# Kernel tuning notes

Measured on AMD Instinct MI355X. Metric: run time of the kernel, lower is better.

The kernel has to match this reference:

```python
import jax, jax.numpy as jnp
import numpy as np

B, S, G, E = 2048, 32768, 4096, 1024  # batch, source_size, n_groups(target_size), embeddings_size


def setup_inputs() -> dict:
    key = jax.random.key(0)
    k_x, k_w, k_we, k_perm = jax.random.split(key, 4)
    x = jax.random.normal(k_x, (B, S), dtype=jnp.float32)
    W = jax.random.normal(k_w, (E, G), dtype=jnp.float32) * 0.02  # Linear(target_size -> embed, no bias)
    # per-element weights for 'w_sum' groups (concatenated Linear(group_size,1) weights)
    w_elem = jax.random.normal(k_we, (S,), dtype=jnp.float32) * 0.1
    perm = jax.random.permutation(k_perm, S).astype(jnp.int32)
    # ragged group boundaries: n_groups groups, each size >= 1, summing to S
    rng = np.random.default_rng(0)
    cuts = np.sort(rng.choice(np.arange(1, S), G - 1, replace=False))
    sizes = np.diff(np.concatenate([[0], cuts, [S]]))
    segment_ids = jnp.asarray(np.repeat(np.arange(G), sizes), dtype=jnp.int32)
    # aggregation type per group: 0='sum', 1='or', 2='w_sum'
    agg_type = jnp.asarray(rng.integers(0, 3, G), dtype=jnp.int32)
    return {"x": x, "W": W, "w_elem": w_elem, "perm": perm,
            "segment_ids": segment_ids, "agg_type": agg_type}


def reference(x, W, w_elem, perm, segment_ids, agg_type):
    # gather via groups_permute
    xp = x[:, perm]  # [B, S]
    # fused ragged per-group reductions, segment axis first: [S, B] -> [G, B]
    xt = xp.T
    seg_sum = jax.ops.segment_sum(xt, segment_ids, num_segments=G)              # jnp.sum per group
    seg_wsum = jax.ops.segment_sum(xt * w_elem[:, None], segment_ids, num_segments=G)  # Linear(g,1) per group
    seg_nnz = jax.ops.segment_sum((xt != 0).astype(x.dtype), segment_ids, num_segments=G)
    seg_or = (seg_nnz > 0).astype(x.dtype)                                       # jnp.any per group (bool -> float on hstack)
    a = agg_type[:, None]
    y = jnp.where(a == 0, seg_sum, jnp.where(a == 1, seg_or, seg_wsum)).T        # [B, G]
    # relu + Linear(target_size -> embeddings_size, no bias)
    return jnp.einsum('bg,eg->be', jax.nn.relu(y), W)
```

## Files before the change

### kernel.cpp

```cpp
#include <hip/hip_runtime.h>
#include <hip/hip_bf16.h>

#define B_DIM 2048
#define S_DIM 32768
#define G_DIM 4096
#define E_DIM 1024

typedef __bf16 bf16x8 __attribute__((ext_vector_type(8)));
typedef __bf16 bf16x4 __attribute__((ext_vector_type(4)));
typedef float f32x4 __attribute__((ext_vector_type(4)));
typedef unsigned short ushort8 __attribute__((ext_vector_type(8)));

__device__ __forceinline__ unsigned short f2bf(float f) {
  unsigned int u = __builtin_bit_cast(unsigned int, f);
  u += 0x7FFFu + ((u >> 16) & 1u);
  return (unsigned short)(u >> 16);
}

__device__ __forceinline__ void async16(void* lds, const void* g) {
  __builtin_amdgcn_global_load_lds(
      (const __attribute__((address_space(1))) unsigned int*)g,
      (__attribute__((address_space(3))) unsigned int*)lds, 16, 0, 0);
}

__device__ __forceinline__ void lds_add(float* p, float v) {
  unsigned off = (unsigned)(size_t)(__attribute__((address_space(3))) float*)p;
  asm volatile("ds_add_f32 %0, %1" :: "v"(off), "v"(v));
}

__global__ __launch_bounds__(256) void setup_meta(
    const float* __restrict__ w_elem, const int* __restrict__ perm,
    const int* __restrict__ segid, const int* __restrict__ agg,
    unsigned* __restrict__ meta1) {
  int s = blockIdx.x * 256 + threadIdx.x;
  if (s >= S_DIM) return;
  int g = segid[s];
  int a = agg[g];
  float cm = (a == 0) ? 1.0f : (a == 2 ? w_elem[s] : 0.0f);
  meta1[s] = (unsigned)perm[s] | (a == 1 ? 0x8000u : 0u) |
             ((unsigned)f2bf(cm) << 16);
}

__global__ __launch_bounds__(256) void setup_runs(
    const int* __restrict__ segid, unsigned* __restrict__ metaH,
    unsigned short* __restrict__ metaG) {
  int t = blockIdx.x * 256 + threadIdx.x;
  if (t >= S_DIM / 32) return;
  int s0 = t * 32;
  int prev = (s0 == 0) ? -1 : segid[s0 - 1];
  unsigned m = 0;
#pragma unroll
  for (int c = 0; c < 8; ++c) {
    int4 gw = *reinterpret_cast<const int4*>(segid + s0 + c * 4);
    if (gw.x != prev) m |= 1u << (c * 4 + 0);
    if (gw.y != gw.x) m |= 1u << (c * 4 + 1);
    if (gw.z != gw.y) m |= 1u << (c * 4 + 2);
    if (gw.w != gw.z) m |= 1u << (c * 4 + 3);
    prev = gw.w;
  }
  metaH[t] = m;
  metaG[t] = (unsigned short)segid[s0];
}

__global__ __launch_bounds__(256) void conv_w(const float* __restrict__ W,
                                              unsigned short* __restrict__ Wb) {
  size_t i = ((size_t)blockIdx.x * 256 + threadIdx.x) * 4;
  float4 v = *reinterpret_cast<const float4*>(W + i);
  ushort4 o;
  o.x = f2bf(v.x);
  o.y = f2bf(v.y);
  o.z = f2bf(v.z);
  o.w = f2bf(v.w);
  *reinterpret_cast<ushort4*>(Wb + i) = o;
}

__global__ __launch_bounds__(1024, 8) void seg_reduce(
    const float* __restrict__ x, const unsigned* __restrict__ meta1,
    const unsigned* __restrict__ metaH, const unsigned short* __restrict__ metaG,
    const int* __restrict__ agg, unsigned short* __restrict__ y) {
  __shared__ unsigned short xrow[S_DIM];
  __shared__ float acc[G_DIM];
  const int t = threadIdx.x;
  const int b = blockIdx.x;

#pragma unroll
  for (int i = 0; i < G_DIM / 1024; ++i) acc[t + i * 1024] = 0.0f;

  const float4* xg = reinterpret_cast<const float4*>(x + (size_t)b * S_DIM);
#pragma unroll
  for (int i = 0; i < S_DIM / 4 / 1024; ++i) {
    float4 v = xg[i * 1024 + t];
    bf16x4 h;
    h.x = (__bf16)v.x;
    h.y = (__bf16)v.y;
    h.z = (__bf16)v.z;
    h.w = (__bf16)v.w;
    *reinterpret_cast<bf16x4*>(&xrow[(i * 1024 + t) * 4]) = h;
  }
  __syncthreads();

  const int s0 = t * 32;
  const unsigned mrun = metaH[t];
  const bool firstPlain = (mrun & 1u) != 0;
  int g = metaG[t];
  float sum = 0.0f;
  int nflush = 0;

  for (int h = 0; h < 2; ++h) {
    const int sb = s0 + h * 16;
    uint4 ma = *reinterpret_cast<const uint4*>(meta1 + sb);
    uint4 mb = *reinterpret_cast<const uint4*>(meta1 + sb + 4);
    uint4 mc = *reinterpret_cast<const uint4*>(meta1 + sb + 8);
    uint4 md = *reinterpret_cast<const uint4*>(meta1 + sb + 12);
    unsigned m[16] = {ma.x, ma.y, ma.z, ma.w, mb.x, mb.y, mb.z, mb.w,
                      mc.x, mc.y, mc.z, mc.w, md.x, md.y, md.z, md.w};
    unsigned short xu[16];
#pragma unroll
    for (int j = 0; j < 16; ++j) xu[j] = xrow[m[j] & 0x7FFF];
    const unsigned mh = mrun >> (h * 16);
#pragma unroll
    for (int j = 0; j < 16; ++j) {
      if (h + j > 0 && (mh & (1u << j))) {
        if (nflush == 0 && !firstPlain) {
          lds_add(&acc[g], sum);
        } else {
          acc[g] = sum;
        }
        ++nflush;
        sum = 0.0f;
        ++g;
      }
      float xv = __builtin_bit_cast(float, (unsigned)xu[j] << 16);
      float cm = __builtin_bit_cast(float, m[j] & 0xFFFF0000u);
      float v = (m[j] & 0x8000u) ? (xu[j] ? 1.0f : 0.0f) : xv * cm;
      sum += v;
    }
  }
  lds_add(&acc[g], sum);

  asm volatile("s_waitcnt lgkmcnt(0)" ::: "memory");
  __syncthreads();

#pragma unroll
  for (int i = 0; i < G_DIM / 1024; ++i) {
    int g2 = t + i * 1024;
    float v = acc[g2];
    if (agg[g2] == 1) v = (v > 0.0f) ? 1.0f : 0.0f;
    v = fmaxf(v, 0.0f);
    y[(size_t)b * G_DIM + g2] = f2bf(v);
  }
}

__global__ __launch_bounds__(256) void gemm_bt(
    const unsigned short* __restrict__ A,
    const unsigned short* __restrict__ Bw,
    float* __restrict__ C) {
  __shared__ __align__(16) unsigned short As[64 * 64];
  __shared__ __align__(16) unsigned short Bs[64 * 64];
  const int t = threadIdx.x;
  const int lane = t & 63;
  const int wid = t >> 6;
  const int wr = wid >> 1;
  const int wc = wid & 1;
  const int row0 = blockIdx.y * 64;
  const int col0 = blockIdx.x * 64;

  const int r_ = t >> 3;
  const int s_ = t & 7;
  const int ksw = (s_ ^ (r_ & 7)) * 8;
  const unsigned short* Ag0 = A + (size_t)(row0 + r_) * G_DIM + ksw;
  const unsigned short* Ag1 = A + (size_t)(row0 + r_ + 32) * G_DIM + ksw;
  const unsigned short* Bg0 = Bw + (size_t)(col0 + r_) * G_DIM + ksw;
  const unsigned short* Bg1 = Bw + (size_t)(col0 + r_ + 32) * G_DIM + ksw;

  char* AsB = (char*)As;
  char* BsB = (char*)Bs;
  char* dA0 = AsB + wid * 1024;
  char* dA1 = AsB + 4096 + wid * 1024;
  char* dB0 = BsB + wid * 1024;
  char* dB1 = BsB + 4096 + wid * 1024;

  const int lm = lane & 15;
  const int lk = lane >> 4;

  f32x4 acc[2][2] = {};

  for (int kt = 0; kt < G_DIM; kt += 64) {
    async16(dA0, Ag0 + kt);
    async16(dA1, Ag1 + kt);
    async16(dB0, Bg0 + kt);
    async16(dB1, Bg1 + kt);
    __syncthreads();
#pragma unroll
    for (int kk = 0; kk < 2; ++kk) {
      bf16x8 af[2], bfr[2];
#pragma unroll
      for (int m = 0; m < 2; ++m) {
        int row = wr * 32 + m * 16 + lm;
        int slot = (kk * 4 + lk) ^ (row & 7);
        af[m] = *(const bf16x8*)(AsB + row * 128 + slot * 16);
      }
#pragma unroll
      for (int n = 0; n < 2; ++n) {
        int row = wc * 32 + n * 16 + lm;
        int slot = (kk * 4 + lk) ^ (row & 7);
        bfr[n] = *(const bf16x8*)(BsB + row * 128 + slot * 16);
      }
#pragma unroll
      for (int m = 0; m < 2; ++m)
#pragma unroll
        for (int n = 0; n < 2; ++n)
          acc[m][n] = __builtin_amdgcn_mfma_f32_16x16x32_bf16(af[m], bfr[n],
                                                              acc[m][n], 0, 0, 0);
    }
    __syncthreads();
  }

#pragma unroll
  for (int m = 0; m < 2; ++m) {
    int r = row0 + wr * 32 + m * 16 + lk * 4;
#pragma unroll
    for (int n = 0; n < 2; ++n) {
      int c = col0 + wc * 32 + n * 16 + lm;
#pragma unroll
      for (int q = 0; q < 4; ++q) {
        C[(size_t)(r + q) * E_DIM + c] = acc[m][n][q];
      }
    }
  }
}

extern "C" void kernel_launch(void* const* d_in, const int* in_sizes, int n_in,
                              void* d_out, int out_size, void* d_ws, size_t ws_size,
                              hipStream_t stream) {
  const float* x = (const float*)d_in[0];
  const float* W = (const float*)d_in[1];
  const float* w_elem = (const float*)d_in[2];
  const int* perm = (const int*)d_in[3];
  const int* segid = (const int*)d_in[4];
  const int* agg = (const int*)d_in[5];
  float* out = (float*)d_out;

  char* ws = (char*)d_ws;
  unsigned short* y = (unsigned short*)ws;
  unsigned short* Wb =
      (unsigned short*)(ws + (size_t)B_DIM * G_DIM * 2);
  unsigned* meta1 =
      (unsigned*)(ws + (size_t)B_DIM * G_DIM * 2 + (size_t)E_DIM * G_DIM * 2);
  unsigned* metaH = (unsigned*)((char*)meta1 + (size_t)S_DIM * 4);
  unsigned short* metaG = (unsigned short*)((char*)metaH + (S_DIM / 32) * 4);

  hipLaunchKernelGGL(setup_meta, dim3(S_DIM / 256), dim3(256), 0, stream,
                     w_elem, perm, segid, agg, meta1);
  hipLaunchKernelGGL(setup_runs, dim3((S_DIM / 32) / 256), dim3(256), 0,
                     stream, segid, metaH, metaG);
  hipLaunchKernelGGL(conv_w, dim3((E_DIM * G_DIM / 4) / 256), dim3(256), 0,
                     stream, W, Wb);
  hipLaunchKernelGGL(seg_reduce, dim3(B_DIM), dim3(1024), 0, stream, x, meta1,
                     metaH, metaG, agg, y);
  hipLaunchKernelGGL(gemm_bt, dim3(E_DIM / 64, B_DIM / 64), dim3(256), 0,
                     stream, y, Wb, out);
}
```

Baseline: 137.1 us.

## Process two batch rows per seg_reduce block to amortize metadata and gathers

```diff
diff --git a/kernel.cpp b/kernel.cpp
--- a/kernel.cpp
+++ b/kernel.cpp
@@ -9,7 +9,6 @@
 typedef __bf16 bf16x8 __attribute__((ext_vector_type(8)));
 typedef __bf16 bf16x4 __attribute__((ext_vector_type(4)));
 typedef float f32x4 __attribute__((ext_vector_type(4)));
-typedef unsigned short ushort8 __attribute__((ext_vector_type(8)));
 
 __device__ __forceinline__ unsigned short f2bf(float f) {
   unsigned int u = __builtin_bit_cast(unsigned int, f);
@@ -74,28 +73,37 @@
   *reinterpret_cast<ushort4*>(Wb + i) = o;
 }
 
-__global__ __launch_bounds__(1024, 8) void seg_reduce(
+__global__ __launch_bounds__(1024, 4) void seg_reduce(
     const float* __restrict__ x, const unsigned* __restrict__ meta1,
     const unsigned* __restrict__ metaH, const unsigned short* __restrict__ metaG,
     const int* __restrict__ agg, unsigned short* __restrict__ y) {
-  __shared__ unsigned short xrow[S_DIM];
-  __shared__ float acc[G_DIM];
+  __shared__ unsigned xrow2[S_DIM];
+  __shared__ float acc2[2 * G_DIM];
   const int t = threadIdx.x;
-  const int b = blockIdx.x;
-
-#pragma unroll
-  for (int i = 0; i < G_DIM / 1024; ++i) acc[t + i * 1024] = 0.0f;
-
-  const float4* xg = reinterpret_cast<const float4*>(x + (size_t)b * S_DIM);
+  const int b0 = blockIdx.x * 2;
+
+#pragma unroll
+  for (int i = 0; i < (2 * G_DIM) / (1024 * 4); ++i)
+    *reinterpret_cast<float4*>(&acc2[(i * 1024 + t) * 4]) =
+        make_float4(0.f, 0.f, 0.f, 0.f);
+
+  const float4* xg0 = reinterpret_cast<const float4*>(x + (size_t)b0 * S_DIM);
+  const float4* xg1 =
+      reinterpret_cast<const float4*>(x + (size_t)(b0 + 1) * S_DIM);
 #pragma unroll
   for (int i = 0; i < S_DIM / 4 / 1024; ++i) {
-    float4 v = xg[i * 1024 + t];
-    bf16x4 h;
-    h.x = (__bf16)v.x;
-    h.y = (__bf16)v.y;
-    h.z = (__bf16)v.z;
-    h.w = (__bf16)v.w;
-    *reinterpret_cast<bf16x4*>(&xrow[(i * 1024 + t) * 4]) = h;
+    float4 v0 = xg0[i * 1024 + t];
+    float4 v1 = xg1[i * 1024 + t];
+    uint4 p;
+    p.x = (unsigned)__builtin_bit_cast(unsigned short, (__bf16)v0.x) |
+          ((unsigned)__builtin_bit_cast(unsigned short, (__bf16)v1.x) << 16);
+    p.y = (unsigned)__builtin_bit_cast(unsigned short, (__bf16)v0.y) |
+          ((unsigned)__builtin_bit_cast(unsigned short, (__bf16)v1.y) << 16);
+    p.z = (unsigned)__builtin_bit_cast(unsigned short, (__bf16)v0.z) |
+          ((unsigned)__builtin_bit_cast(unsigned short, (__bf16)v1.z) << 16);
+    p.w = (unsigned)__builtin_bit_cast(unsigned short, (__bf16)v0.w) |
+          ((unsigned)__builtin_bit_cast(unsigned short, (__bf16)v1.w) << 16);
+    *reinterpret_cast<uint4*>(&xrow2[(i * 1024 + t) * 4]) = p;
   }
   __syncthreads();
 
@@ -103,7 +111,7 @@
   const unsigned mrun = metaH[t];
   const bool firstPlain = (mrun & 1u) != 0;
   int g = metaG[t];
-  float sum = 0.0f;
+  float sum0 = 0.0f, sum1 = 0.0f;
   int nflush = 0;
 
   for (int h = 0; h < 2; ++h) {
@@ -114,29 +122,39 @@
     uint4 md = *reinterpret_cast<const uint4*>(meta1 + sb + 12);
     unsigned m[16] = {ma.x, ma.y, ma.z, ma.w, mb.x, mb.y, mb.z, mb.w,
                       mc.x, mc.y, mc.z, mc.w, md.x, md.y, md.z, md.w};
-    unsigned short xu[16];
-#pragma unroll
-    for (int j = 0; j < 16; ++j) xu[j] = xrow[m[j] & 0x7FFF];
+    unsigned xu[16];
+#pragma unroll
+    for (int j = 0; j < 16; ++j) xu[j] = xrow2[m[j] & 0x7FFF];
     const unsigned mh = mrun >> (h * 16);
 #pragma unroll
     for (int j = 0; j < 16; ++j) {
       if (h + j > 0 && (mh & (1u << j))) {
         if (nflush == 0 && !firstPlain) {
-          lds_add(&acc[g], sum);
+          lds_add(&acc2[2 * g], sum0);
+          lds_add(&acc2[2 * g + 1], sum1);
         } else {
-          acc[g] = sum;
+          *reinterpret_cast<float2*>(&acc2[2 * g]) =
+              make_float2(sum0, sum1);
         }
         ++nflush;
-        sum = 0.0f;
+        sum0 = 0.0f;
+        sum1 = 0.0f;
         ++g;
       }
-      float xv = __builtin_bit_cast(float, (unsigned)xu[j] << 16);
+      float x0 = __builtin_bit_cast(float, xu[j] << 16);
+      float x1 = __builtin_bit_cast(float, xu[j] & 0xFFFF0000u);
       float cm = __builtin_bit_cast(float, m[j] & 0xFFFF0000u);
-      float v = (m[j] & 0x8000u) ? (xu[j] ? 1.0f : 0.0f) : xv * cm;
-      sum += v;
-    }
-  }
-  lds_add(&acc[g], sum);
+      if (m[j] & 0x8000u) {
+        sum0 += (xu[j] & 0xFFFFu) ? 1.0f : 0.0f;
+        sum1 += (xu[j] >> 16) ? 1.0f : 0.0f;
+      } else {
+        sum0 += x0 * cm;
+        sum1 += x1 * cm;
+      }
+    }
+  }
+  lds_add(&acc2[2 * g], sum0);
+  lds_add(&acc2[2 * g + 1], sum1);
 
   asm volatile("s_waitcnt lgkmcnt(0)" ::: "memory");
   __syncthreads();
@@ -144,10 +162,16 @@
 #pragma unroll
   for (int i = 0; i < G_DIM / 1024; ++i) {
     int g2 = t + i * 1024;
-    float v = acc[g2];
-    if (agg[g2] == 1) v = (v > 0.0f) ? 1.0f : 0.0f;
-    v = fmaxf(v, 0.0f);
-    y[(size_t)b * G_DIM + g2] = f2bf(v);
+    float2 vv = *reinterpret_cast<const float2*>(&acc2[2 * g2]);
+    float v0 = vv.x, v1 = vv.y;
+    if (agg[g2] == 1) {
+      v0 = (v0 > 0.0f) ? 1.0f : 0.0f;
+      v1 = (v1 > 0.0f) ? 1.0f : 0.0f;
+    }
+    v0 = fmaxf(v0, 0.0f);
+    v1 = fmaxf(v1, 0.0f);
+    y[(size_t)b0 * G_DIM + g2] = f2bf(v0);
+    y[(size_t)(b0 + 1) * G_DIM + g2] = f2bf(v1);
   }
 }
 
@@ -256,8 +280,8 @@
                      stream, segid, metaH, metaG);
   hipLaunchKernelGGL(conv_w, dim3((E_DIM * G_DIM / 4) / 256), dim3(256), 0,
                      stream, W, Wb);
-  hipLaunchKernelGGL(seg_reduce, dim3(B_DIM), dim3(1024), 0, stream, x, meta1,
-                     metaH, metaG, agg, y);
+  hipLaunchKernelGGL(seg_reduce, dim3(B_DIM / 2), dim3(1024), 0, stream, x,
+                     meta1, metaH, metaG, agg, y);
   hipLaunchKernelGGL(gemm_bt, dim3(E_DIM / 64, B_DIM / 64), dim3(256), 0,
                      stream, y, Wb, out);
 }
```

New measurement: 150.7 us. 9.9% more time.

## Process four batch rows per seg_reduce block with register-prefetched next row

Applied to the files above, without the earlier changes.

```diff
diff --git a/kernel.cpp b/kernel.cpp
--- a/kernel.cpp
+++ b/kernel.cpp
@@ -5,11 +5,10 @@
 #define S_DIM 32768
 #define G_DIM 4096
 #define E_DIM 1024
+#define ROWS_PER_BLK 4
 
 typedef __bf16 bf16x8 __attribute__((ext_vector_type(8)));
-typedef __bf16 bf16x4 __attribute__((ext_vector_type(4)));
 typedef float f32x4 __attribute__((ext_vector_type(4)));
-typedef unsigned short ushort8 __attribute__((ext_vector_type(8)));
 
 __device__ __forceinline__ unsigned short f2bf(float f) {
   unsigned int u = __builtin_bit_cast(unsigned int, f);
@@ -26,6 +25,15 @@
 __device__ __forceinline__ void lds_add(float* p, float v) {
   unsigned off = (unsigned)(size_t)(__attribute__((address_space(3))) float*)p;
   asm volatile("ds_add_f32 %0, %1" :: "v"(off), "v"(v));
+}
+
+__device__ __forceinline__ uint2 pack4bf(float4 v) {
+  uint2 r;
+  r.x = (unsigned)__builtin_bit_cast(unsigned short, (__bf16)v.x) |
+        ((unsigned)__builtin_bit_cast(unsigned short, (__bf16)v.y) << 16);
+  r.y = (unsigned)__builtin_bit_cast(unsigned short, (__bf16)v.z) |
+        ((unsigned)__builtin_bit_cast(unsigned short, (__bf16)v.w) << 16);
+  return r;
 }
 
 __global__ __launch_bounds__(256) void setup_meta(
@@ -81,73 +89,101 @@
   __shared__ unsigned short xrow[S_DIM];
   __shared__ float acc[G_DIM];
   const int t = threadIdx.x;
-  const int b = blockIdx.x;
-
-#pragma unroll
-  for (int i = 0; i < G_DIM / 1024; ++i) acc[t + i * 1024] = 0.0f;
-
-  const float4* xg = reinterpret_cast<const float4*>(x + (size_t)b * S_DIM);
-#pragma unroll
-  for (int i = 0; i < S_DIM / 4 / 1024; ++i) {
-    float4 v = xg[i * 1024 + t];
-    bf16x4 h;
-    h.x = (__bf16)v.x;
-    h.y = (__bf16)v.y;
-    h.z = (__bf16)v.z;
-    h.w = (__bf16)v.w;
-    *reinterpret_cast<bf16x4*>(&xrow[(i * 1024 + t) * 4]) = h;
-  }
-  __syncthreads();
+  const int b0 = blockIdx.x * ROWS_PER_BLK;
 
   const int s0 = t * 32;
   const unsigned mrun = metaH[t];
   const bool firstPlain = (mrun & 1u) != 0;
-  int g = metaG[t];
-  float sum = 0.0f;
-  int nflush = 0;
-
-  for (int h = 0; h < 2; ++h) {
-    const int sb = s0 + h * 16;
-    uint4 ma = *reinterpret_cast<const uint4*>(meta1 + sb);
-    uint4 mb = *reinterpret_cast<const uint4*>(meta1 + sb + 4);
-    uint4 mc = *reinterpret_cast<const uint4*>(meta1 + sb + 8);
-    uint4 md = *reinterpret_cast<const uint4*>(meta1 + sb + 12);
-    unsigned m[16] = {ma.x, ma.y, ma.z, ma.w, mb.x, mb.y, mb.z, mb.w,
-                      mc.x, mc.y, mc.z, mc.w, md.x, md.y, md.z, md.w};
-    unsigned short xu[16];
-#pragma unroll
-    for (int j = 0; j < 16; ++j) xu[j] = xrow[m[j] & 0x7FFF];
-    const unsigned mh = mrun >> (h * 16);
-#pragma unroll
-    for (int j = 0; j < 16; ++j) {
-      if (h + j > 0 && (mh & (1u << j))) {
-        if (nflush == 0 && !firstPlain) {
-          lds_add(&acc[g], sum);
-        } else {
-          acc[g] = sum;
+  const unsigned g0 = metaG[t];
+  const int a0 = agg[t];
+  const int a1 = agg[t + 1024];
+  const int a2 = agg[t + 2048];
+  const int a3 = agg[t + 3072];
+
+#pragma unroll
+  for (int i = 0; i < G_DIM / 1024; ++i) acc[t + i * 1024] = 0.0f;
+
+  {
+    const float4* xg = reinterpret_cast<const float4*>(x + (size_t)b0 * S_DIM);
+#pragma unroll
+    for (int k = 0; k < 8; ++k) {
+      uint2 p = pack4bf(xg[k * 1024 + t]);
+      *reinterpret_cast<uint2*>(&xrow[(k * 1024 + t) * 4]) = p;
+    }
+  }
+  __syncthreads();
+
+  for (int i = 0; i < ROWS_PER_BLK; ++i) {
+    uint2 sv[8];
+    if (i < ROWS_PER_BLK - 1) {
+      const float4* xgn =
+          reinterpret_cast<const float4*>(x + (size_t)(b0 + i + 1) * S_DIM);
+#pragma unroll
+      for (int k = 0; k < 8; ++k) sv[k] = pack4bf(xgn[k * 1024 + t]);
+    }
+
+    unsigned g = g0;
+    float sum = 0.0f;
+    int nflush = 0;
+#pragma unroll
+    for (int q = 0; q < 4; ++q) {
+      const int sb = s0 + q * 8;
+      uint4 ma = *reinterpret_cast<const uint4*>(meta1 + sb);
+      uint4 mb = *reinterpret_cast<const uint4*>(meta1 + sb + 4);
+      unsigned m[8] = {ma.x, ma.y, ma.z, ma.w, mb.x, mb.y, mb.z, mb.w};
+      unsigned short xu[8];
+#pragma unroll
+      for (int j = 0; j < 8; ++j) xu[j] = xrow[m[j] & 0x7FFF];
+      const unsigned mh = mrun >> (q * 8);
+#pragma unroll
+      for (int j = 0; j < 8; ++j) {
+        if (q * 8 + j > 0 && (mh & (1u << j))) {
+          if (nflush == 0 && !firstPlain) {
+            lds_add(&acc[g], sum);
+          } else {
+            acc[g] = sum;
+          }
+          ++nflush;
+          sum = 0.0f;
+          ++g;
         }
-        ++nflush;
-        sum = 0.0f;
-        ++g;
-      }
-      float xv = __builtin_bit_cast(float, (unsigned)xu[j] << 16);
-      float cm = __builtin_bit_cast(float, m[j] & 0xFFFF0000u);
-      float v = (m[j] & 0x8000u) ? (xu[j] ? 1.0f : 0.0f) : xv * cm;
-      sum += v;
-    }
-  }
-  lds_add(&acc[g], sum);
-
-  asm volatile("s_waitcnt lgkmcnt(0)" ::: "memory");
-  __syncthreads();
-
-#pragma unroll
-  for (int i = 0; i < G_DIM / 1024; ++i) {
-    int g2 = t + i * 1024;
-    float v = acc[g2];
-    if (agg[g2] == 1) v = (v > 0.0f) ? 1.0f : 0.0f;
-    v = fmaxf(v, 0.0f);
-    y[(size_t)b * G_DIM + g2] = f2bf(v);
+        float xv = __builtin_bit_cast(float, (unsigned)xu[j] << 16);
+        float cm = __builtin_bit_cast(float, m[j] & 0xFFFF0000u);
+        float v = (m[j] & 0x8000u) ? (xu[j] ? 1.0f : 0.0f) : xv * cm;
+        sum += v;
+      }
+    }
+    lds_add(&acc[g], sum);
+
+    asm volatile("s_waitcnt lgkmcnt(0)" ::: "memory");
+    __syncthreads();
+
+    if (i < ROWS_PER_BLK - 1) {
+#pragma unroll
+      for (int k = 0; k < 8; ++k)
+        *reinterpret_cast<uint2*>(&xrow[(k * 1024 + t) * 4]) = sv[k];
+    }
+
+    {
+      const size_t yb = (size_t)(b0 + i) * G_DIM;
+      float v0 = acc[t];
+      float v1 = acc[t + 1024];
+      float v2 = acc[t + 2048];
+      float v3 = acc[t + 3072];
+      if (a0 == 1) v0 = (v0 > 0.0f) ? 1.0f : 0.0f;
+      if (a1 == 1) v1 = (v1 > 0.0f) ? 1.0f : 0.0f;
+      if (a2 == 1) v2 = (v2 > 0.0f) ? 1.0f : 0.0f;
+      if (a3 == 1) v3 = (v3 > 0.0f) ? 1.0f : 0.0f;
+      y[yb + t] = f2bf(fmaxf(v0, 0.0f));
+      y[yb + t + 1024] = f2bf(fmaxf(v1, 0.0f));
+      y[yb + t + 2048] = f2bf(fmaxf(v2, 0.0f));
+      y[yb + t + 3072] = f2bf(fmaxf(v3, 0.0f));
+      acc[t] = 0.0f;
+      acc[t + 1024] = 0.0f;
+      acc[t + 2048] = 0.0f;
+      acc[t + 3072] = 0.0f;
+    }
+    __syncthreads();
   }
 }
 
@@ -256,8 +292,8 @@
                      stream, segid, metaH, metaG);
   hipLaunchKernelGGL(conv_w, dim3((E_DIM * G_DIM / 4) / 256), dim3(256), 0,
                      stream, W, Wb);
-  hipLaunchKernelGGL(seg_reduce, dim3(B_DIM), dim3(1024), 0, stream, x, meta1,
-                     metaH, metaG, agg, y);
+  hipLaunchKernelGGL(seg_reduce, dim3(B_DIM / ROWS_PER_BLK), dim3(1024), 0,
+                     stream, x, meta1, metaH, metaG, agg, y);
   hipLaunchKernelGGL(gemm_bt, dim3(E_DIM / 64, B_DIM / 64), dim3(256), 0,
                      stream, y, Wb, out);
 }
```

After: 153.5 us. 1.12x slower.

## Split GEMM along K into four partial products and add reduction kernel

Applied to the files above, without the earlier changes.

```diff
diff --git a/kernel.cpp b/kernel.cpp
--- a/kernel.cpp
+++ b/kernel.cpp
@@ -5,11 +5,11 @@
 #define S_DIM 32768
 #define G_DIM 4096
 #define E_DIM 1024
+#define KSPLIT 4
+#define KCHUNK (G_DIM / KSPLIT)
 
 typedef __bf16 bf16x8 __attribute__((ext_vector_type(8)));
-typedef __bf16 bf16x4 __attribute__((ext_vector_type(4)));
 typedef float f32x4 __attribute__((ext_vector_type(4)));
-typedef unsigned short ushort8 __attribute__((ext_vector_type(8)));
 
 __device__ __forceinline__ unsigned short f2bf(float f) {
   unsigned int u = __builtin_bit_cast(unsigned int, f);
@@ -90,12 +90,14 @@
 #pragma unroll
   for (int i = 0; i < S_DIM / 4 / 1024; ++i) {
     float4 v = xg[i * 1024 + t];
-    bf16x4 h;
-    h.x = (__bf16)v.x;
-    h.y = (__bf16)v.y;
-    h.z = (__bf16)v.z;
-    h.w = (__bf16)v.w;
-    *reinterpret_cast<bf16x4*>(&xrow[(i * 1024 + t) * 4]) = h;
+    unsigned short h0 = __builtin_bit_cast(unsigned short, (__bf16)v.x);
+    unsigned short h1 = __builtin_bit_cast(unsigned short, (__bf16)v.y);
+    unsigned short h2 = __builtin_bit_cast(unsigned short, (__bf16)v.z);
+    unsigned short h3 = __builtin_bit_cast(unsigned short, (__bf16)v.w);
+    uint2 p;
+    p.x = (unsigned)h0 | ((unsigned)h1 << 16);
+    p.y = (unsigned)h2 | ((unsigned)h3 << 16);
+    *reinterpret_cast<uint2*>(&xrow[(i * 1024 + t) * 4]) = p;
   }
   __syncthreads();
 
@@ -154,7 +156,7 @@
 __global__ __launch_bounds__(256) void gemm_bt(
     const unsigned short* __restrict__ A,
     const unsigned short* __restrict__ Bw,
-    float* __restrict__ C) {
+    float* __restrict__ part) {
   __shared__ __align__(16) unsigned short As[64 * 64];
   __shared__ __align__(16) unsigned short Bs[64 * 64];
   const int t = threadIdx.x;
@@ -164,6 +166,7 @@
   const int wc = wid & 1;
   const int row0 = blockIdx.y * 64;
   const int col0 = blockIdx.x * 64;
+  const int kc = blockIdx.z;
 
   const int r_ = t >> 3;
   const int s_ = t & 7;
@@ -185,7 +188,7 @@
 
   f32x4 acc[2][2] = {};
 
-  for (int kt = 0; kt < G_DIM; kt += 64) {
+  for (int kt = kc * KCHUNK; kt < (kc + 1) * KCHUNK; kt += 64) {
     async16(dA0, Ag0 + kt);
     async16(dA1, Ag1 + kt);
     async16(dB0, Bg0 + kt);
@@ -216,6 +219,7 @@
     __syncthreads();
   }
 
+  float* P = part + (size_t)kc * B_DIM * E_DIM;
 #pragma unroll
   for (int m = 0; m < 2; ++m) {
     int r = row0 + wr * 32 + m * 16 + lk * 4;
@@ -224,10 +228,26 @@
       int c = col0 + wc * 32 + n * 16 + lm;
 #pragma unroll
       for (int q = 0; q < 4; ++q) {
-        C[(size_t)(r + q) * E_DIM + c] = acc[m][n][q];
+        P[(size_t)(r + q) * E_DIM + c] = acc[m][n][q];
       }
     }
   }
+}
+
+__global__ __launch_bounds__(256) void reduce_part(
+    const float* __restrict__ part, float* __restrict__ C) {
+  const size_t i = ((size_t)blockIdx.x * 256 + threadIdx.x) * 4;
+  const size_t n = (size_t)B_DIM * E_DIM;
+  float4 v0 = *reinterpret_cast<const float4*>(part + i);
+  float4 v1 = *reinterpret_cast<const float4*>(part + n + i);
+  float4 v2 = *reinterpret_cast<const float4*>(part + 2 * n + i);
+  float4 v3 = *reinterpret_cast<const float4*>(part + 3 * n + i);
+  float4 o;
+  o.x = (v0.x + v1.x) + (v2.x + v3.x);
+  o.y = (v0.y + v1.y) + (v2.y + v3.y);
+  o.z = (v0.z + v1.z) + (v2.z + v3.z);
+  o.w = (v0.w + v1.w) + (v2.w + v3.w);
+  *reinterpret_cast<float4*>(C + i) = o;
 }
 
 extern "C" void kernel_launch(void* const* d_in, const int* in_sizes, int n_in,
@@ -245,8 +265,10 @@
   unsigned short* y = (unsigned short*)ws;
   unsigned short* Wb =
       (unsigned short*)(ws + (size_t)B_DIM * G_DIM * 2);
-  unsigned* meta1 =
-      (unsigned*)(ws + (size_t)B_DIM * G_DIM * 2 + (size_t)E_DIM * G_DIM * 2);
+  float* part = (float*)(ws + (size_t)B_DIM * G_DIM * 2 +
+                         (size_t)E_DIM * G_DIM * 2);
+  unsigned* meta1 = (unsigned*)((char*)part +
+                                (size_t)KSPLIT * B_DIM * E_DIM * 4);
   unsigned* metaH = (unsigned*)((char*)meta1 + (size_t)S_DIM * 4);
   unsigned short* metaG = (unsigned short*)((char*)metaH + (S_DIM / 32) * 4);
 
@@ -258,6 +280,9 @@
                      stream, W, Wb);
   hipLaunchKernelGGL(seg_reduce, dim3(B_DIM), dim3(1024), 0, stream, x, meta1,
                      metaH, metaG, agg, y);
-  hipLaunchKernelGGL(gemm_bt, dim3(E_DIM / 64, B_DIM / 64), dim3(256), 0,
-                     stream, y, Wb, out);
-}
+  hipLaunchKernelGGL(gemm_bt, dim3(E_DIM / 64, B_DIM / 64, KSPLIT), dim3(256),
+                     0, stream, y, Wb, part);
+  hipLaunchKernelGGL(reduce_part,
+                     dim3(((size_t)B_DIM * E_DIM / 4) / 256), dim3(256), 0,
+                     stream, part, out);
+}
```

After: 130.0 us. -5.2%, faster.
